# Kernel optimization log

Hardware: AMD Instinct MI355X
Metric: run time of the kernel (lower is better)

## Reference

```python
import jax, jax.numpy as jnp
import numpy as np

B, D, H, T, S, FD = 4, 1024, 12, 32, 32, 64
NUM_BUCKETS = 32
MAX_BUCKET = NUM_BUCKETS // 2            # 16
MIN_BUCKET = MAX_BUCKET - NUM_BUCKETS + 1  # -15


def setup_inputs() -> dict:
    key = jax.random.key(0)
    k1, k2, k3 = jax.random.split(key, 3)
    qk = jax.random.normal(k1, (B, D, H, T, FD), dtype=jnp.float32)
    # raw (unclamped) pairwise frame distances, exercises both clamp bounds
    pairwise_distances = jax.random.randint(k2, (B, T, S), -40, 40, dtype=jnp.int32)
    lookup_table_weight = jax.random.normal(k3, (NUM_BUCKETS, H, FD), dtype=jnp.float32) * 0.02
    return {"qk": qk, "pairwise_distances": pairwise_distances,
            "lookup_table_weight": lookup_table_weight}


def reference(qk, pairwise_distances, lookup_table_weight):
    # clamp distances to bucket range [MIN_BUCKET, MAX_BUCKET]
    pd = jnp.clip(pairwise_distances, MIN_BUCKET, MAX_BUCKET)
    # torch negative indexing wraps: idx in [0, NUM_BUCKETS)
    idx = jnp.where(pd < 0, pd + NUM_BUCKETS, pd)
    R = lookup_table_weight[idx]  # [B, T, S, H, F]
    # mode == 'qk': per-(b,t,s) dot of qk features with gathered RPE vectors
    return jnp.einsum('bdhtf,btshf->bdhts', qk, R)  # [B, D, H, T, S]
```

## Files before the change

### kernel.cpp

```cpp
#include <hip/hip_runtime.h>
#include <hip/hip_bf16.h>

constexpr int Bc = 4, Dc = 1024, Hc = 12, Tc = 32, Sc = 32, Fc = 64;
constexpr int DCH = 16;
constexpr int HB  = 6;
constexpr int STEPS = 2 * HB;
constexpr int QPITCH = 1032;

typedef __bf16 bf16x8 __attribute__((ext_vector_type(8)));
typedef __bf16 bf16x4 __attribute__((ext_vector_type(4)));
typedef float  f32x4  __attribute__((ext_vector_type(4)));

__global__ __launch_bounds__(512, 4) void rpe_staged(
    const float* __restrict__ qk,
    const int*   __restrict__ pdist,
    const float* __restrict__ lut,
    float*       __restrict__ out)
{
    __shared__ __align__(16) __bf16 Qs[2][DCH][QPITCH];
    __shared__ __align__(16) __bf16 Rl[2][32][72];
    __shared__ unsigned char idxl[Tc][Sc];

    const int bid = blockIdx.x;
    const int hh  = bid & 1;
    const int dc  = (bid >> 1) & 63;
    const int b   = bid >> 7;
    const int d0  = dc * DCH;
    const int h0  = hh * HB;

    const int tid = threadIdx.x;

    const int sd = tid >> 5;
    const int sc = tid & 31;
    const float* qsrc = qk + (size_t)((b * Dc + d0 + sd) * Hc) * Tc * Fc + sc * 8;

    const int rbu = tid >> 4;
    const int rf0 = (tid & 15) * 4;

    if (tid < 256) {
        const int t  = tid >> 3;
        const int s0 = (tid & 7) * 4;
        const int4 p = *reinterpret_cast<const int4*>(pdist + (b * Tc + t) * Sc + s0);
        uchar4 u; int v;
        v = p.x; v = v < -15 ? -15 : (v > 16 ? 16 : v); u.x = (unsigned char)(v < 0 ? v + 32 : v);
        v = p.y; v = v < -15 ? -15 : (v > 16 ? 16 : v); u.y = (unsigned char)(v < 0 ? v + 32 : v);
        v = p.z; v = v < -15 ? -15 : (v > 16 ? 16 : v); u.z = (unsigned char)(v < 0 ? v + 32 : v);
        v = p.w; v = v < -15 ? -15 : (v > 16 ? 16 : v); u.w = (unsigned char)(v < 0 ? v + 32 : v);
        *reinterpret_cast<uchar4*>(&idxl[t][s0]) = u;
    }
    f32x4 g[4][2];
    f32x4 rg;
    {
        const float* qp = qsrc + h0 * 2048;
        #pragma unroll
        for (int j = 0; j < 4; ++j) {
            g[j][0] = *reinterpret_cast<const f32x4*>(qp + j * 256);
            g[j][1] = *reinterpret_cast<const f32x4*>(qp + j * 256 + 4);
        }
        rg = *reinterpret_cast<const f32x4*>(lut + (rbu * Hc + h0) * Fc + rf0);
    }
    #pragma unroll
    for (int j = 0; j < 4; ++j) {
        bf16x8 w;
        #pragma unroll
        for (int k = 0; k < 4; ++k) { w[k] = (__bf16)g[j][0][k]; w[k + 4] = (__bf16)g[j][1][k]; }
        *reinterpret_cast<bf16x8*>(&Qs[0][sd][sc * 8 + j * 256]) = w;
    }
    {
        bf16x4 w4;
        #pragma unroll
        for (int k = 0; k < 4; ++k) w4[k] = (__bf16)rg[k];
        *reinterpret_cast<bf16x4*>(&Rl[0][rbu][rf0]) = w4;
    }
    __syncthreads();

    const int lane = tid & 63;
    const int wv   = tid >> 6;
    const int r16  = lane & 15;
    const int grp  = lane >> 4;
    float* obase = out + (size_t)((b * Dc + d0 + r16) * Hc) * Tc * Sc;

    #pragma unroll 2
    for (int s = 0; s < STEPS; ++s) {
        const int buf   = s & 1;
        const int hl    = s >> 1;
        const int thalf = s & 1;
        const int h     = h0 + hl;

        if (s + 1 < STEPS) {
            const float* qp = qsrc + (h0 + ((s + 1) >> 1)) * 2048 + ((s + 1) & 1) * 1024;
            #pragma unroll
            for (int j = 0; j < 4; ++j) {
                g[j][0] = *reinterpret_cast<const f32x4*>(qp + j * 256);
                g[j][1] = *reinterpret_cast<const f32x4*>(qp + j * 256 + 4);
            }
            if (s & 1)
                rg = *reinterpret_cast<const f32x4*>(
                    lut + (rbu * Hc + h0 + ((s + 1) >> 1)) * Fc + rf0);
        }

        #pragma unroll
        for (int tt = 0; tt < 2; ++tt) {
            const int tl = wv * 2 + tt;
            const int tg = thalf * 16 + tl;
            const int i0 = idxl[tg][r16];
            const int i1 = idxl[tg][16 + r16];
            bf16x8 a00 = *reinterpret_cast<const bf16x8*>(&Rl[hl & 1][i0][grp * 8]);
            bf16x8 a01 = *reinterpret_cast<const bf16x8*>(&Rl[hl & 1][i0][32 + grp * 8]);
            bf16x8 a10 = *reinterpret_cast<const bf16x8*>(&Rl[hl & 1][i1][grp * 8]);
            bf16x8 a11 = *reinterpret_cast<const bf16x8*>(&Rl[hl & 1][i1][32 + grp * 8]);
            bf16x8 bf0 = *reinterpret_cast<const bf16x8*>(&Qs[buf][r16][tl * 64 + grp * 8]);
            bf16x8 bf1 = *reinterpret_cast<const bf16x8*>(&Qs[buf][r16][tl * 64 + 32 + grp * 8]);

            f32x4 acc0 = {0.f, 0.f, 0.f, 0.f};
            f32x4 acc1 = {0.f, 0.f, 0.f, 0.f};
            acc0 = __builtin_amdgcn_mfma_f32_16x16x32_bf16(a00, bf0, acc0, 0, 0, 0);
            acc0 = __builtin_amdgcn_mfma_f32_16x16x32_bf16(a01, bf1, acc0, 0, 0, 0);
            acc1 = __builtin_amdgcn_mfma_f32_16x16x32_bf16(a10, bf0, acc1, 0, 0, 0);
            acc1 = __builtin_amdgcn_mfma_f32_16x16x32_bf16(a11, bf1, acc1, 0, 0, 0);

            float* op = obase + h * (Tc * Sc) + tg * Sc;
            *reinterpret_cast<f32x4*>(op + grp * 4)      = acc0;
            *reinterpret_cast<f32x4*>(op + 16 + grp * 4) = acc1;
        }

        if (s + 1 < STEPS) {
            #pragma unroll
            for (int j = 0; j < 4; ++j) {
                bf16x8 w;
                #pragma unroll
                for (int k = 0; k < 4; ++k) { w[k] = (__bf16)g[j][0][k]; w[k + 4] = (__bf16)g[j][1][k]; }
                *reinterpret_cast<bf16x8*>(&Qs[buf ^ 1][sd][sc * 8 + j * 256]) = w;
            }
            if (s & 1) {
                bf16x4 w4;
                #pragma unroll
                for (int k = 0; k < 4; ++k) w4[k] = (__bf16)rg[k];
                *reinterpret_cast<bf16x4*>(&Rl[((s + 1) >> 1) & 1][rbu][rf0]) = w4;
            }
        }
        __syncthreads();
    }
}

extern "C" void kernel_launch(void* const* d_in, const int* in_sizes, int n_in,
                              void* d_out, int out_size, void* d_ws, size_t ws_size,
                              hipStream_t stream) {
    const float* qk    = (const float*)d_in[0];
    const int*   pdist = (const int*)d_in[1];
    const float* lut   = (const float*)d_in[2];
    float*       out   = (float*)d_out;

    const int grid = Bc * 64 * 2;
    rpe_staged<<<grid, 512, 0, stream>>>(qk, pdist, lut, out);
}
```

Baseline: 124.8 us.

## Stage output tile in shared memory for coalesced stores, single-buffer Q

Result: no change. 123.6 us (-1.0%).

```diff
diff --git a/kernel.cpp b/kernel.cpp
--- a/kernel.cpp
+++ b/kernel.cpp
@@ -5,21 +5,23 @@
 constexpr int DCH = 16;
 constexpr int HB  = 6;
 constexpr int STEPS = 2 * HB;
-constexpr int QPITCH = 1032;
+constexpr int QP  = 1032;
+constexpr int OP  = 516;
 
 typedef __bf16 bf16x8 __attribute__((ext_vector_type(8)));
 typedef __bf16 bf16x4 __attribute__((ext_vector_type(4)));
 typedef float  f32x4  __attribute__((ext_vector_type(4)));
 
-__global__ __launch_bounds__(512, 4) void rpe_staged(
+__global__ __launch_bounds__(512, 4) void rpe_ws(
     const float* __restrict__ qk,
     const int*   __restrict__ pdist,
     const float* __restrict__ lut,
     float*       __restrict__ out)
 {
-    __shared__ __align__(16) __bf16 Qs[2][DCH][QPITCH];
+    __shared__ __align__(16) __bf16 Qs[DCH][QP];
     __shared__ __align__(16) __bf16 Rl[2][32][72];
     __shared__ unsigned char idxl[Tc][Sc];
+    __shared__ __align__(16) float  Os[DCH][OP];
 
     const int bid = blockIdx.x;
     const int hh  = bid & 1;
@@ -49,7 +51,6 @@
         *reinterpret_cast<uchar4*>(&idxl[t][s0]) = u;
     }
     f32x4 g[4][2];
-    f32x4 rg;
     {
         const float* qp = qsrc + h0 * 2048;
         #pragma unroll
@@ -57,20 +58,18 @@
             g[j][0] = *reinterpret_cast<const f32x4*>(qp + j * 256);
             g[j][1] = *reinterpret_cast<const f32x4*>(qp + j * 256 + 4);
         }
-        rg = *reinterpret_cast<const f32x4*>(lut + (rbu * Hc + h0) * Fc + rf0);
+        f32x4 rg = *reinterpret_cast<const f32x4*>(lut + (rbu * Hc + h0) * Fc + rf0);
+        bf16x4 w4;
+        #pragma unroll
+        for (int k = 0; k < 4; ++k) w4[k] = (__bf16)rg[k];
+        *reinterpret_cast<bf16x4*>(&Rl[0][rbu][rf0]) = w4;
     }
     #pragma unroll
     for (int j = 0; j < 4; ++j) {
         bf16x8 w;
         #pragma unroll
         for (int k = 0; k < 4; ++k) { w[k] = (__bf16)g[j][0][k]; w[k + 4] = (__bf16)g[j][1][k]; }
-        *reinterpret_cast<bf16x8*>(&Qs[0][sd][sc * 8 + j * 256]) = w;
-    }
-    {
-        bf16x4 w4;
-        #pragma unroll
-        for (int k = 0; k < 4; ++k) w4[k] = (__bf16)rg[k];
-        *reinterpret_cast<bf16x4*>(&Rl[0][rbu][rf0]) = w4;
+        *reinterpret_cast<bf16x8*>(&Qs[sd][sc * 8 + j * 256]) = w;
     }
     __syncthreads();
 
@@ -78,11 +77,8 @@
     const int wv   = tid >> 6;
     const int r16  = lane & 15;
     const int grp  = lane >> 4;
-    float* obase = out + (size_t)((b * Dc + d0 + r16) * Hc) * Tc * Sc;
 
-    #pragma unroll 2
     for (int s = 0; s < STEPS; ++s) {
-        const int buf   = s & 1;
         const int hl    = s >> 1;
         const int thalf = s & 1;
         const int h     = h0 + hl;
@@ -94,9 +90,6 @@
                 g[j][0] = *reinterpret_cast<const f32x4*>(qp + j * 256);
                 g[j][1] = *reinterpret_cast<const f32x4*>(qp + j * 256 + 4);
             }
-            if (s & 1)
-                rg = *reinterpret_cast<const f32x4*>(
-                    lut + (rbu * Hc + h0 + ((s + 1) >> 1)) * Fc + rf0);
         }
 
         #pragma unroll
@@ -109,8 +102,8 @@
             bf16x8 a01 = *reinterpret_cast<const bf16x8*>(&Rl[hl & 1][i0][32 + grp * 8]);
             bf16x8 a10 = *reinterpret_cast<const bf16x8*>(&Rl[hl & 1][i1][grp * 8]);
             bf16x8 a11 = *reinterpret_cast<const bf16x8*>(&Rl[hl & 1][i1][32 + grp * 8]);
-            bf16x8 bf0 = *reinterpret_cast<const bf16x8*>(&Qs[buf][r16][tl * 64 + grp * 8]);
-            bf16x8 bf1 = *reinterpret_cast<const bf16x8*>(&Qs[buf][r16][tl * 64 + 32 + grp * 8]);
+            bf16x8 bf0 = *reinterpret_cast<const bf16x8*>(&Qs[r16][tl * 64 + grp * 8]);
+            bf16x8 bf1 = *reinterpret_cast<const bf16x8*>(&Qs[r16][tl * 64 + 32 + grp * 8]);
 
             f32x4 acc0 = {0.f, 0.f, 0.f, 0.f};
             f32x4 acc1 = {0.f, 0.f, 0.f, 0.f};
@@ -119,10 +112,10 @@
             acc1 = __builtin_amdgcn_mfma_f32_16x16x32_bf16(a10, bf0, acc1, 0, 0, 0);
             acc1 = __builtin_amdgcn_mfma_f32_16x16x32_bf16(a11, bf1, acc1, 0, 0, 0);
 
-            float* op = obase + h * (Tc * Sc) + tg * Sc;
-            *reinterpret_cast<f32x4*>(op + grp * 4)      = acc0;
-            *reinterpret_cast<f32x4*>(op + 16 + grp * 4) = acc1;
+            *reinterpret_cast<f32x4*>(&Os[r16][tl * 32 + grp * 4])      = acc0;
+            *reinterpret_cast<f32x4*>(&Os[r16][tl * 32 + 16 + grp * 4]) = acc1;
         }
+        __syncthreads();
 
         if (s + 1 < STEPS) {
             #pragma unroll
@@ -130,13 +123,26 @@
                 bf16x8 w;
                 #pragma unroll
                 for (int k = 0; k < 4; ++k) { w[k] = (__bf16)g[j][0][k]; w[k + 4] = (__bf16)g[j][1][k]; }
-                *reinterpret_cast<bf16x8*>(&Qs[buf ^ 1][sd][sc * 8 + j * 256]) = w;
+                *reinterpret_cast<bf16x8*>(&Qs[sd][sc * 8 + j * 256]) = w;
             }
             if (s & 1) {
+                f32x4 rg = *reinterpret_cast<const f32x4*>(
+                    lut + (rbu * Hc + h0 + hl + 1) * Fc + rf0);
                 bf16x4 w4;
                 #pragma unroll
                 for (int k = 0; k < 4; ++k) w4[k] = (__bf16)rg[k];
-                *reinterpret_cast<bf16x4*>(&Rl[((s + 1) >> 1) & 1][rbu][rf0]) = w4;
+                *reinterpret_cast<bf16x4*>(&Rl[(hl + 1) & 1][rbu][rf0]) = w4;
+            }
+        }
+        {
+            const int od = tid >> 5;
+            const int oc = tid & 31;
+            float* op = out + ((size_t)(b * Dc + d0 + od) * Hc + h) * Tc * Sc
+                            + thalf * 512;
+            #pragma unroll
+            for (int j = 0; j < 4; ++j) {
+                f32x4 v = *reinterpret_cast<const f32x4*>(&Os[od][oc * 4 + j * 128]);
+                *reinterpret_cast<f32x4*>(op + oc * 4 + j * 128) = v;
             }
         }
         __syncthreads();
@@ -152,5 +158,5 @@
     float*       out   = (float*)d_out;
 
     const int grid = Bc * 64 * 2;
-    rpe_staged<<<grid, 512, 0, stream>>>(qk, pdist, lut, out);
+    rpe_ws<<<grid, 512, 0, stream>>>(qk, pdist, lut, out);
 }
```

## Stage MFMA outputs through LDS for coalesced stores, one block per d-chunk

Applied to the files above, without the earlier changes.

Result: no change. 126.0 us (+0.9%).

```diff
diff --git a/kernel.cpp b/kernel.cpp
--- a/kernel.cpp
+++ b/kernel.cpp
@@ -2,40 +2,40 @@
 #include <hip/hip_bf16.h>
 
 constexpr int Bc = 4, Dc = 1024, Hc = 12, Tc = 32, Sc = 32, Fc = 64;
-constexpr int DCH = 16;
-constexpr int HB  = 6;
-constexpr int STEPS = 2 * HB;
-constexpr int QPITCH = 1032;
+constexpr int QP = 1032;
+constexpr int OP = 516;
+constexpr int STEPS = 24;
 
 typedef __bf16 bf16x8 __attribute__((ext_vector_type(8)));
 typedef __bf16 bf16x4 __attribute__((ext_vector_type(4)));
 typedef float  f32x4  __attribute__((ext_vector_type(4)));
 
-__global__ __launch_bounds__(512, 4) void rpe_staged(
+__global__ __launch_bounds__(1024, 4) void rpe_stream(
     const float* __restrict__ qk,
     const int*   __restrict__ pdist,
     const float* __restrict__ lut,
     float*       __restrict__ out)
 {
-    __shared__ __align__(16) __bf16 Qs[2][DCH][QPITCH];
+    __shared__ __align__(16) __bf16 Qs[2][16][QP];
+    __shared__ __align__(16) float  Os[2][16][OP];
     __shared__ __align__(16) __bf16 Rl[2][32][72];
     __shared__ unsigned char idxl[Tc][Sc];
 
     const int bid = blockIdx.x;
-    const int hh  = bid & 1;
-    const int dc  = (bid >> 1) & 63;
-    const int b   = bid >> 7;
-    const int d0  = dc * DCH;
-    const int h0  = hh * HB;
+    const int dc  = bid & 63;
+    const int b   = bid >> 6;
+    const int d0  = dc * 16;
 
     const int tid = threadIdx.x;
-
-    const int sd = tid >> 5;
-    const int sc = tid & 31;
-    const float* qsrc = qk + (size_t)((b * Dc + d0 + sd) * Hc) * Tc * Fc + sc * 8;
-
+    const int w   = tid >> 6;
+    const int l   = tid & 63;
+    const int r16 = l & 15;
+    const int grp = l >> 4;
     const int rbu = tid >> 4;
     const int rf0 = (tid & 15) * 4;
+
+    const float* qsrc  = qk  + (size_t)((b * Dc + d0 + w) * Hc) * Tc * Fc + l * 4;
+    float*       obase = out + (size_t)((b * Dc + d0 + w) * Hc) * Tc * Sc;
 
     if (tid < 256) {
         const int t  = tid >> 3;
@@ -48,69 +48,52 @@
         v = p.w; v = v < -15 ? -15 : (v > 16 ? 16 : v); u.w = (unsigned char)(v < 0 ? v + 32 : v);
         *reinterpret_cast<uchar4*>(&idxl[t][s0]) = u;
     }
-    f32x4 g[4][2];
-    f32x4 rg;
-    {
-        const float* qp = qsrc + h0 * 2048;
-        #pragma unroll
-        for (int j = 0; j < 4; ++j) {
-            g[j][0] = *reinterpret_cast<const f32x4*>(qp + j * 256);
-            g[j][1] = *reinterpret_cast<const f32x4*>(qp + j * 256 + 4);
-        }
-        rg = *reinterpret_cast<const f32x4*>(lut + (rbu * Hc + h0) * Fc + rf0);
-    }
-    #pragma unroll
-    for (int j = 0; j < 4; ++j) {
-        bf16x8 w;
-        #pragma unroll
-        for (int k = 0; k < 4; ++k) { w[k] = (__bf16)g[j][0][k]; w[k + 4] = (__bf16)g[j][1][k]; }
-        *reinterpret_cast<bf16x8*>(&Qs[0][sd][sc * 8 + j * 256]) = w;
-    }
-    {
+    if (tid < 512) {
+        f32x4 rg = *reinterpret_cast<const f32x4*>(lut + (rbu * Hc) * Fc + rf0);
         bf16x4 w4;
         #pragma unroll
         for (int k = 0; k < 4; ++k) w4[k] = (__bf16)rg[k];
         *reinterpret_cast<bf16x4*>(&Rl[0][rbu][rf0]) = w4;
     }
+    #pragma unroll
+    for (int k = 0; k < 4; ++k) {
+        f32x4 v = *reinterpret_cast<const f32x4*>(qsrc + k * 256);
+        bf16x4 q4;
+        #pragma unroll
+        for (int j = 0; j < 4; ++j) q4[j] = (__bf16)v[j];
+        *reinterpret_cast<bf16x4*>(&Qs[0][w][k * 256 + l * 4]) = q4;
+    }
     __syncthreads();
-
-    const int lane = tid & 63;
-    const int wv   = tid >> 6;
-    const int r16  = lane & 15;
-    const int grp  = lane >> 4;
-    float* obase = out + (size_t)((b * Dc + d0 + r16) * Hc) * Tc * Sc;
 
     #pragma unroll 2
     for (int s = 0; s < STEPS; ++s) {
-        const int buf   = s & 1;
-        const int hl    = s >> 1;
-        const int thalf = s & 1;
-        const int h     = h0 + hl;
+        const int cur = s & 1;
+        const int h   = s >> 1;
+        const int th  = s & 1;
 
-        if (s + 1 < STEPS) {
-            const float* qp = qsrc + (h0 + ((s + 1) >> 1)) * 2048 + ((s + 1) & 1) * 1024;
-            #pragma unroll
-            for (int j = 0; j < 4; ++j) {
-                g[j][0] = *reinterpret_cast<const f32x4*>(qp + j * 256);
-                g[j][1] = *reinterpret_cast<const f32x4*>(qp + j * 256 + 4);
-            }
-            if (s & 1)
+        f32x4 g0, g1, g2, g3, rg;
+        if (s < STEPS - 1) {
+            const float* qp = qsrc + ((s + 1) >> 1) * 2048 + ((s + 1) & 1) * 1024;
+            g0 = *reinterpret_cast<const f32x4*>(qp);
+            g1 = *reinterpret_cast<const f32x4*>(qp + 256);
+            g2 = *reinterpret_cast<const f32x4*>(qp + 512);
+            g3 = *reinterpret_cast<const f32x4*>(qp + 768);
+            if ((s & 1) && tid < 512)
                 rg = *reinterpret_cast<const f32x4*>(
-                    lut + (rbu * Hc + h0 + ((s + 1) >> 1)) * Fc + rf0);
+                    lut + (rbu * Hc + h + 1) * Fc + rf0);
         }
 
-        #pragma unroll
-        for (int tt = 0; tt < 2; ++tt) {
-            const int tl = wv * 2 + tt;
-            const int tg = thalf * 16 + tl;
+        {
+            const int tg = th * 16 + w;
             const int i0 = idxl[tg][r16];
             const int i1 = idxl[tg][16 + r16];
-            bf16x8 a00 = *reinterpret_cast<const bf16x8*>(&Rl[hl & 1][i0][grp * 8]);
-            bf16x8 a01 = *reinterpret_cast<const bf16x8*>(&Rl[hl & 1][i0][32 + grp * 8]);
-            bf16x8 a10 = *reinterpret_cast<const bf16x8*>(&Rl[hl & 1][i1][grp * 8]);
-            bf16x8 a11 = *reinterpret_cast<const bf16x8*>(&Rl[hl & 1][i1][32 + grp * 8]);
-            bf16x8 bf0 = *reinterpret_cast<const bf16x8*>(&Qs[buf][r16][tl * 64 + grp * 8]);
-            bf16x8 bf1 = *reinterpret_cast<const bf16x8*>(&Qs[buf][r16][tl * 64 + 32 + grp * 8]);
+            const int hp = h & 1;
+            bf16x8 a00 = *reinterpret_cast<const bf16x8*>(&Rl[hp][i0][grp * 8]);
+            bf16x8 a01 = *reinterpret_cast<const bf16x8*>(&Rl[hp][i0][32 + grp * 8]);
+            bf16x8 a10 = *reinterpret_cast<const bf16x8*>(&Rl[hp][i1][grp * 8]);
+            bf16x8 a11 = *reinterpret_cast<const bf16x8*>(&Rl[hp][i1][32 + grp * 8]);
+            bf16x8 bf0 = *reinterpret_cast<const bf16x8*>(&Qs[cur][r16][w * 64 + grp * 8]);
+            bf16x8 bf1 = *reinterpret_cast<const bf16x8*>(&Qs[cur][r16][w * 64 + 32 + grp * 8]);
 
             f32x4 acc0 = {0.f, 0.f, 0.f, 0.f};
             f32x4 acc1 = {0.f, 0.f, 0.f, 0.f};
@@ -119,27 +102,50 @@
             acc1 = __builtin_amdgcn_mfma_f32_16x16x32_bf16(a10, bf0, acc1, 0, 0, 0);
             acc1 = __builtin_amdgcn_mfma_f32_16x16x32_bf16(a11, bf1, acc1, 0, 0, 0);
 
-            float* op = obase + h * (Tc * Sc) + tg * Sc;
-            *reinterpret_cast<f32x4*>(op + grp * 4)      = acc0;
-            *reinterpret_cast<f32x4*>(op + 16 + grp * 4) = acc1;
+            *reinterpret_cast<f32x4*>(&Os[cur][r16][w * 32 + grp * 4])      = acc0;
+            *reinterpret_cast<f32x4*>(&Os[cur][r16][w * 32 + 16 + grp * 4]) = acc1;
         }
 
-        if (s + 1 < STEPS) {
+        if (s > 0) {
+            const int sp = s - 1;
+            float* op = obase + (sp >> 1) * 1024 + (sp & 1) * 512 + l * 4;
+            f32x4 v0 = *reinterpret_cast<const f32x4*>(&Os[cur ^ 1][w][l * 4]);
+            f32x4 v1 = *reinterpret_cast<const f32x4*>(&Os[cur ^ 1][w][256 + l * 4]);
+            *reinterpret_cast<f32x4*>(op)       = v0;
+            *reinterpret_cast<f32x4*>(op + 256) = v1;
+        }
+
+        if (s < STEPS - 1) {
+            bf16x4 q4;
             #pragma unroll
-            for (int j = 0; j < 4; ++j) {
-                bf16x8 w;
-                #pragma unroll
-                for (int k = 0; k < 4; ++k) { w[k] = (__bf16)g[j][0][k]; w[k + 4] = (__bf16)g[j][1][k]; }
-                *reinterpret_cast<bf16x8*>(&Qs[buf ^ 1][sd][sc * 8 + j * 256]) = w;
-            }
-            if (s & 1) {
+            for (int j = 0; j < 4; ++j) q4[j] = (__bf16)g0[j];
+            *reinterpret_cast<bf16x4*>(&Qs[cur ^ 1][w][l * 4]) = q4;
+            #pragma unroll
+            for (int j = 0; j < 4; ++j) q4[j] = (__bf16)g1[j];
+            *reinterpret_cast<bf16x4*>(&Qs[cur ^ 1][w][256 + l * 4]) = q4;
+            #pragma unroll
+            for (int j = 0; j < 4; ++j) q4[j] = (__bf16)g2[j];
+            *reinterpret_cast<bf16x4*>(&Qs[cur ^ 1][w][512 + l * 4]) = q4;
+            #pragma unroll
+            for (int j = 0; j < 4; ++j) q4[j] = (__bf16)g3[j];
+            *reinterpret_cast<bf16x4*>(&Qs[cur ^ 1][w][768 + l * 4]) = q4;
+
+            if ((s & 1) && tid < 512) {
                 bf16x4 w4;
                 #pragma unroll
                 for (int k = 0; k < 4; ++k) w4[k] = (__bf16)rg[k];
-                *reinterpret_cast<bf16x4*>(&Rl[((s + 1) >> 1) & 1][rbu][rf0]) = w4;
+                *reinterpret_cast<bf16x4*>(&Rl[(h + 1) & 1][rbu][rf0]) = w4;
             }
         }
         __syncthreads();
+    }
+
+    {
+        float* op = obase + 11 * 1024 + 512 + l * 4;
+        f32x4 v0 = *reinterpret_cast<const f32x4*>(&Os[1][w][l * 4]);
+        f32x4 v1 = *reinterpret_cast<const f32x4*>(&Os[1][w][256 + l * 4]);
+        *reinterpret_cast<f32x4*>(op)       = v0;
+        *reinterpret_cast<f32x4*>(op + 256) = v1;
     }
 }
 
@@ -151,6 +157,6 @@
     const float* lut   = (const float*)d_in[2];
     float*       out   = (float*)d_out;
 
-    const int grid = Bc * 64 * 2;
-    rpe_staged<<<grid, 512, 0, stream>>>(qk, pdist, lut, out);
+    const int grid = Bc * 64;
+    rpe_stream<<<grid, 1024, 0, stream>>>(qk, pdist, lut, out);
 }
```
